# Performance work log

Hardware: AMD Instinct MI355X
Metric: run time of the kernel (lower is better)

Reference implementation:

```python
import jax
import jax.numpy as jnp
from jax import lax
import numpy as np

MAX_Q = 127.0  # 2**(8-1) - 1, signed int8 symmetric


def setup_inputs() -> dict:
    key = jax.random.key(0)
    kx, kw, kb = jax.random.split(key, 3)
    x = jax.random.normal(kx, (32, 8, 384, 384), dtype=jnp.float32)
    weight = jax.random.normal(kw, (8, 8, 3, 3), dtype=jnp.float32) * 0.1
    bias = jax.random.normal(kb, (8,), dtype=jnp.float32) * 0.01
    return {"x": x, "weight": weight, "bias": bias}


def _quantize(v, scale):
    # per-tensor symmetric int8 quantization: round, clip to [-127, 127]
    return jnp.clip(jnp.round(v * scale), -MAX_Q, MAX_Q)


def reference(x, weight, bias):
    # calibrated per-tensor amax == abs-max of the tensor
    sx = MAX_Q / jnp.max(jnp.abs(x))
    sw = MAX_Q / jnp.max(jnp.abs(weight))
    qx = _quantize(x, sx)       # int values in [-127,127], kept in fp32 (exact)
    qw = _quantize(weight, sw)
    # exact int conv (systolic kernel, use_exact=True): products <= 127^2,
    # K = 8*3*3 = 72 terms -> max |accum| ~ 1.16e6 << 2^24, exact in fp32.
    out_i32 = lax.conv_general_dilated(
        qx, qw,
        window_strides=(1, 1),
        padding=[(1, 1), (1, 1)],
        lhs_dilation=(1, 1),
        rhs_dilation=(1, 1),
        dimension_numbers=("NCHW", "OIHW", "NCHW"),
    )
    out = out_i32 / (sx * sw)   # dequantize: scale = (127/amax_x)*(127/amax_w)
    return out + bias[None, :, None, None]
```

## Files before the change

kernel.cpp:

```cpp
#include <hip/hip_runtime.h>

#define PLANE (384 * 384)
#define TH 16
#define TW 64
#define TROWS 18
#define TCOLS 66

typedef float f4_t __attribute__((ext_vector_type(4)));

#if __has_builtin(__builtin_amdgcn_sdot4)
__device__ __forceinline__ int sdot4(int a, int b, int c) {
    return __builtin_amdgcn_sdot4(a, b, c, false);
}
#else
__device__ __forceinline__ int sdot4(int a, int b, int c) {
    #pragma unroll
    for (int i = 0; i < 4; ++i)
        c += ((a << (24 - 8 * i)) >> 24) * ((b << (24 - 8 * i)) >> 24);
    return c;
}
#endif

__global__ __launch_bounds__(256) void amax_kernel(
    const float* __restrict__ x, const float* __restrict__ w,
    unsigned int* __restrict__ ws)
{
    __shared__ float red[4];
    const float4* x4 = (const float4*)x;
    const int tid = blockIdx.x * 256 + threadIdx.x;

    float m = 0.f;
    #pragma unroll
    for (int i = 0; i < 18; ++i) {
        float4 v = x4[tid + i * 524288];
        m = fmaxf(m, fmaxf(fmaxf(fabsf(v.x), fabsf(v.y)),
                           fmaxf(fabsf(v.z), fabsf(v.w))));
    }
    #pragma unroll
    for (int off = 32; off > 0; off >>= 1)
        m = fmaxf(m, __shfl_down(m, off, 64));
    if ((threadIdx.x & 63) == 0) red[threadIdx.x >> 6] = m;
    __syncthreads();
    if (threadIdx.x == 0) {
        float bm = fmaxf(fmaxf(red[0], red[1]), fmaxf(red[2], red[3]));
        atomicMax(&ws[0], __float_as_uint(bm));
    }

    if (blockIdx.x == 0) {
        float mw = 0.f;
        for (int j = threadIdx.x; j < 576; j += 256)
            mw = fmaxf(mw, fabsf(w[j]));
        #pragma unroll
        for (int off = 32; off > 0; off >>= 1)
            mw = fmaxf(mw, __shfl_down(mw, off, 64));
        if ((threadIdx.x & 63) == 0)
            atomicMax(&ws[1], __float_as_uint(mw));
    }
}

__global__ __launch_bounds__(256) void conv_kernel(
    const float* __restrict__ x, const float* __restrict__ w,
    const float* __restrict__ bias, const unsigned int* __restrict__ ws,
    float* __restrict__ out)
{
    __shared__ __align__(16) unsigned sIn[TROWS * TCOLS * 2];
    __shared__ __align__(16) unsigned sWq[9 * 8 * 2];
    __shared__ float sB[8];

    const float amax_x = __uint_as_float(ws[0]);
    const float amax_w = __uint_as_float(ws[1]);
    const float s_x = 127.0f / amax_x;
    const float s_w = 127.0f / amax_w;
    const float inv = 1.0f / (s_x * s_w);

    const int bid = blockIdx.x;
    const int bx = bid % 6;
    const int by = (bid / 6) % 24;
    const int n  = bid / (6 * 24);
    const int h0 = by * TH;
    const int w0 = bx * TW;
    const int tid = threadIdx.x;

    if (tid < 144) {
        int h = tid & 1, k = (tid >> 1) & 7, p = tid >> 4;
        unsigned pk = 0;
        #pragma unroll
        for (int j = 0; j < 4; ++j) {
            int c = 4 * h + j;
            float qv = fminf(fmaxf(rintf(w[k * 72 + c * 9 + p] * s_w), -127.f), 127.f);
            int qi = (int)qv;
            pk |= ((unsigned)(qi & 0xff)) << (8 * j);
        }
        sWq[p * 16 + k * 2 + h] = pk;
    }
    if (tid < 8) sB[tid] = bias[tid];

    const float* xn = x + (long)n * 8 * PLANE;

    for (int task = tid; task < 288; task += 256) {
        int yy = task >> 4;
        int g  = task & 15;
        int gy = h0 - 1 + yy;
        bool rowok = ((unsigned)gy < 384u);
        const float* rp = xn + (long)gy * 384 + (w0 + 4 * g);
        unsigned lo[4] = {0, 0, 0, 0}, hi[4] = {0, 0, 0, 0};
        if (rowok) {
            #pragma unroll
            for (int c = 0; c < 8; ++c) {
                f4_t v = *(const f4_t*)(rp + (long)c * PLANE);
                #pragma unroll
                for (int j = 0; j < 4; ++j) {
                    float qv = fminf(fmaxf(rintf(v[j] * s_x), -127.f), 127.f);
                    int qi = (int)qv;
                    unsigned b = ((unsigned)(qi & 0xff)) << (8 * (c & 3));
                    if (c < 4) lo[j] |= b; else hi[j] |= b;
                }
            }
        }
        int q0 = yy * TCOLS + 1 + 4 * g;
        #pragma unroll
        for (int j = 0; j < 4; ++j)
            *(uint2*)&sIn[2 * (q0 + j)] = make_uint2(lo[j], hi[j]);
    }

    if (tid >= 220) {
        int t = tid - 220;
        int yy = t >> 1;
        int xx = (t & 1) ? 65 : 0;
        int gy = h0 - 1 + yy;
        int gx = w0 - 1 + xx;
        bool ok = ((unsigned)gy < 384u) && ((unsigned)gx < 384u);
        long base = (long)gy * 384 + gx;
        unsigned lo = 0, hi = 0;
        if (ok) {
            #pragma unroll
            for (int c = 0; c < 8; ++c) {
                float v = xn[(long)c * PLANE + base];
                float qv = fminf(fmaxf(rintf(v * s_x), -127.f), 127.f);
                int qi = (int)qv;
                if (c < 4) lo |= ((unsigned)(qi & 0xff)) << (8 * c);
                else       hi |= ((unsigned)(qi & 0xff)) << (8 * (c - 4));
            }
        }
        *(uint2*)&sIn[2 * (yy * TCOLS + xx)] = make_uint2(lo, hi);
    }
    __syncthreads();

    const int ty = tid >> 4;
    const int tx = tid & 15;

    int acc[4][8];
    #pragma unroll
    for (int i = 0; i < 4; ++i)
        #pragma unroll
        for (int k = 0; k < 8; ++k) acc[i][k] = 0;

    #pragma unroll
    for (int r = 0; r < 3; ++r) {
        const uint4* ip = (const uint4*)&sIn[((ty + r) * TCOLS + 4 * tx) * 2];
        uint4 i0 = ip[0], i1 = ip[1], i2 = ip[2];
        unsigned d[12] = {i0.x, i0.y, i0.z, i0.w,
                          i1.x, i1.y, i1.z, i1.w,
                          i2.x, i2.y, i2.z, i2.w};
        #pragma unroll
        for (int s = 0; s < 3; ++s) {
            const uint4* wp = (const uint4*)&sWq[(r * 3 + s) * 16];
            uint4 wa = wp[0], wb = wp[1], wc = wp[2], wd = wp[3];
            unsigned wk[16] = {wa.x, wa.y, wa.z, wa.w, wb.x, wb.y, wb.z, wb.w,
                               wc.x, wc.y, wc.z, wc.w, wd.x, wd.y, wd.z, wd.w};
            #pragma unroll
            for (int k = 0; k < 8; ++k)
                #pragma unroll
                for (int i = 0; i < 4; ++i)
                    acc[i][k] = sdot4((int)d[2 * (i + s) + 1], (int)wk[2 * k + 1],
                                sdot4((int)d[2 * (i + s)],     (int)wk[2 * k],
                                      acc[i][k]));
        }
    }

    float* on = out + (long)n * 8 * PLANE + (long)(h0 + ty) * 384 + (w0 + 4 * tx);
    #pragma unroll
    for (int k = 0; k < 8; ++k) {
        f4_t o;
        o.x = fmaf((float)acc[0][k], inv, sB[k]);
        o.y = fmaf((float)acc[1][k], inv, sB[k]);
        o.z = fmaf((float)acc[2][k], inv, sB[k]);
        o.w = fmaf((float)acc[3][k], inv, sB[k]);
        __builtin_nontemporal_store(o, (f4_t*)(on + (long)k * PLANE));
    }
}

extern "C" void kernel_launch(void* const* d_in, const int* in_sizes, int n_in,
                              void* d_out, int out_size, void* d_ws, size_t ws_size,
                              hipStream_t stream) {
    const float* x   = (const float*)d_in[0];
    const float* w   = (const float*)d_in[1];
    const float* b   = (const float*)d_in[2];
    float* out       = (float*)d_out;
    unsigned int* ws = (unsigned int*)d_ws;

    hipMemsetAsync(ws, 0, 2 * sizeof(unsigned int), stream);
    amax_kernel<<<2048, 256, 0, stream>>>(x, w, ws);
    conv_kernel<<<32 * 24 * 6, 256, 0, stream>>>(x, w, b, ws, out);
}
```

Before: 308.9 us.

## Pre-quantize input to packed int8 buffer before the convolution

Adds a separate pass that quantizes the fp32 input once into a packed int8 NHWC-style buffer (8 channels per pixel) in workspace. The convolution then loads compact int8 tiles instead of re-reading and re-quantizing fp32 halos in every block. This cuts conv-stage load bytes and quantization work, but adds a kernel launch and an extra full read of x plus a write of the int8 buffer. It falls back to the original fused kernel if the workspace is too small.

```diff
diff --git a/kernel.cpp b/kernel.cpp
--- a/kernel.cpp
+++ b/kernel.cpp
@@ -58,7 +58,142 @@
     }
 }
 
-__global__ __launch_bounds__(256) void conv_kernel(
+__global__ __launch_bounds__(256) void quant_kernel(
+    const float* __restrict__ x, const unsigned int* __restrict__ ws,
+    unsigned* __restrict__ q)
+{
+    const float s_x = 127.0f / __uint_as_float(ws[0]);
+    const int t = blockIdx.x * 256 + threadIdx.x;
+    const int g = t * 4;
+    const int n = g / PLANE;
+    const int r = g - n * PLANE;
+    const float* xp = x + (long)n * (8 * PLANE) + r;
+
+    unsigned lo[4] = {0, 0, 0, 0}, hi[4] = {0, 0, 0, 0};
+    #pragma unroll
+    for (int c = 0; c < 8; ++c) {
+        f4_t v = *(const f4_t*)(xp + (long)c * PLANE);
+        #pragma unroll
+        for (int j = 0; j < 4; ++j) {
+            float qv = fminf(fmaxf(rintf(v[j] * s_x), -127.f), 127.f);
+            int qi = (int)qv;
+            unsigned b = ((unsigned)(qi & 0xff)) << (8 * (c & 3));
+            if (c < 4) lo[j] |= b; else hi[j] |= b;
+        }
+    }
+    uint4* qp = (uint4*)q + (long)t * 2;
+    qp[0] = make_uint4(lo[0], hi[0], lo[1], hi[1]);
+    qp[1] = make_uint4(lo[2], hi[2], lo[3], hi[3]);
+}
+
+__global__ __launch_bounds__(256) void conv_kernel_q(
+    const unsigned* __restrict__ q, const float* __restrict__ w,
+    const float* __restrict__ bias, const unsigned int* __restrict__ ws,
+    float* __restrict__ out)
+{
+    __shared__ __align__(16) unsigned sIn[TROWS * TCOLS * 2];
+    __shared__ __align__(16) unsigned sWq[9 * 8 * 2];
+    __shared__ float sB[8];
+
+    const float amax_x = __uint_as_float(ws[0]);
+    const float amax_w = __uint_as_float(ws[1]);
+    const float s_x = 127.0f / amax_x;
+    const float s_w = 127.0f / amax_w;
+    const float inv = 1.0f / (s_x * s_w);
+
+    const int bid = blockIdx.x;
+    const int bx = bid % 6;
+    const int by = (bid / 6) % 24;
+    const int n  = bid / (6 * 24);
+    const int h0 = by * TH;
+    const int w0 = bx * TW;
+    const int tid = threadIdx.x;
+
+    if (tid < 144) {
+        int h = tid & 1, k = (tid >> 1) & 7, p = tid >> 4;
+        unsigned pk = 0;
+        #pragma unroll
+        for (int j = 0; j < 4; ++j) {
+            int c = 4 * h + j;
+            float qv = fminf(fmaxf(rintf(w[k * 72 + c * 9 + p] * s_w), -127.f), 127.f);
+            int qi = (int)qv;
+            pk |= ((unsigned)(qi & 0xff)) << (8 * j);
+        }
+        sWq[p * 16 + k * 2 + h] = pk;
+    }
+    if (tid < 8) sB[tid] = bias[tid];
+
+    const unsigned* qn = q + (long)n * PLANE * 2;
+
+    for (int t = tid; t < 576; t += 256) {
+        int yy = t >> 5;
+        int seg = t & 31;
+        int gy = h0 - 1 + yy;
+        uint4 v = make_uint4(0, 0, 0, 0);
+        if ((unsigned)gy < 384u)
+            v = *(const uint4*)(qn + ((long)gy * 384 + (w0 + 2 * seg)) * 2);
+        int p = yy * TCOLS + 1 + 2 * seg;
+        *(uint2*)&sIn[2 * p]     = make_uint2(v.x, v.y);
+        *(uint2*)&sIn[2 * p + 2] = make_uint2(v.z, v.w);
+    }
+    if (tid >= 220) {
+        int t = tid - 220;
+        int yy = t >> 1;
+        int xx = (t & 1) ? 65 : 0;
+        int gy = h0 - 1 + yy;
+        int gx = w0 - 1 + xx;
+        uint2 v = make_uint2(0, 0);
+        if (((unsigned)gy < 384u) && ((unsigned)gx < 384u))
+            v = *(const uint2*)(qn + ((long)gy * 384 + gx) * 2);
+        *(uint2*)&sIn[2 * (yy * TCOLS + xx)] = v;
+    }
+    __syncthreads();
+
+    const int ty = tid >> 4;
+    const int tx = tid & 15;
+
+    int acc[4][8];
+    #pragma unroll
+    for (int i = 0; i < 4; ++i)
+        #pragma unroll
+        for (int k = 0; k < 8; ++k) acc[i][k] = 0;
+
+    #pragma unroll
+    for (int r = 0; r < 3; ++r) {
+        const uint4* ip = (const uint4*)&sIn[((ty + r) * TCOLS + 4 * tx) * 2];
+        uint4 i0 = ip[0], i1 = ip[1], i2 = ip[2];
+        unsigned d[12] = {i0.x, i0.y, i0.z, i0.w,
+                          i1.x, i1.y, i1.z, i1.w,
+                          i2.x, i2.y, i2.z, i2.w};
+        #pragma unroll
+        for (int s = 0; s < 3; ++s) {
+            const uint4* wp = (const uint4*)&sWq[(r * 3 + s) * 16];
+            uint4 wa = wp[0], wb = wp[1], wc = wp[2], wd = wp[3];
+            unsigned wk[16] = {wa.x, wa.y, wa.z, wa.w, wb.x, wb.y, wb.z, wb.w,
+                               wc.x, wc.y, wc.z, wc.w, wd.x, wd.y, wd.z, wd.w};
+            #pragma unroll
+            for (int k = 0; k < 8; ++k)
+                #pragma unroll
+                for (int i = 0; i < 4; ++i)
+                    acc[i][k] = sdot4((int)d[2 * (i + s) + 1], (int)wk[2 * k + 1],
+                                sdot4((int)d[2 * (i + s)],     (int)wk[2 * k],
+                                      acc[i][k]));
+        }
+    }
+
+    float* on = out + (long)n * 8 * PLANE + (long)(h0 + ty) * 384 + (w0 + 4 * tx);
+    #pragma unroll
+    for (int k = 0; k < 8; ++k) {
+        f4_t o;
+        o.x = fmaf((float)acc[0][k], inv, sB[k]);
+        o.y = fmaf((float)acc[1][k], inv, sB[k]);
+        o.z = fmaf((float)acc[2][k], inv, sB[k]);
+        o.w = fmaf((float)acc[3][k], inv, sB[k]);
+        __builtin_nontemporal_store(o, (f4_t*)(on + (long)k * PLANE));
+    }
+}
+
+__global__ __launch_bounds__(256) void conv_kernel_f32(
     const float* __restrict__ x, const float* __restrict__ w,
     const float* __restrict__ bias, const unsigned int* __restrict__ ws,
     float* __restrict__ out)
@@ -201,5 +336,14 @@
 
     hipMemsetAsync(ws, 0, 2 * sizeof(unsigned int), stream);
     amax_kernel<<<2048, 256, 0, stream>>>(x, w, ws);
-    conv_kernel<<<32 * 24 * 6, 256, 0, stream>>>(x, w, b, ws, out);
-}
+
+    const size_t QOFF   = 64;
+    const size_t QBYTES = (size_t)32 * PLANE * 8;
+    if (ws_size >= QOFF + QBYTES) {
+        unsigned* q = (unsigned*)((char*)d_ws + QOFF);
+        quant_kernel<<<4608, 256, 0, stream>>>(x, ws, q);
+        conv_kernel_q<<<4608, 256, 0, stream>>>(q, w, b, ws, out);
+    } else {
+        conv_kernel_f32<<<4608, 256, 0, stream>>>(x, w, b, ws, out);
+    }
+}
```

New measurement: 300.6 us. 1.03x faster.
